# Kernel optimization log

Hardware: AMD Instinct MI355X
Metric: run time of the kernel (lower is better)

## Reference

```python
import jax, jax.numpy as jnp
import numpy as np

N_NODES = 100000
N_EDGES = 1600000
IN_CH = 128
EMB = 64


def _init_linear(key, fan_in, fan_out):
    kw, kb = jax.random.split(key)
    scale = 1.0 / np.sqrt(fan_in)
    W = jax.random.uniform(kw, (fan_in, fan_out), jnp.float32, -scale, scale)
    b = jax.random.uniform(kb, (fan_out,), jnp.float32, -scale, scale)
    return W, b


def setup_inputs() -> dict:
    key = jax.random.key(0)
    ks = jax.random.split(key, 6)
    x = jax.random.normal(ks[0], (N_NODES, IN_CH), jnp.float32)
    edge_index = jax.random.randint(ks[1], (2, N_EDGES), 0, N_NODES)
    batch = jnp.zeros((N_NODES,), jnp.int32)
    # conv1 MLP: in_channels -> 32 -> 64 ; conv2 MLP: 64 -> 64 -> embedding_dim
    W1, b1 = _init_linear(ks[2], IN_CH, 32)
    W2, b2 = _init_linear(ks[3], 32, 64)
    W3, b3 = _init_linear(ks[4], 64, 64)
    W4, b4 = _init_linear(ks[5], 64, EMB)
    return {"x": x, "edge_index": edge_index, "batch": batch,
            "W1": W1, "b1": b1, "W2": W2, "b2": b2,
            "W3": W3, "b3": b3, "W4": W4, "b4": b4}


def _mlp(h, Wa, ba, Wb, bb):
    # PyG MLP: Linear -> act -> Linear (plain last layer)
    return jax.nn.relu(h @ Wa + ba) @ Wb + bb


def _gin_conv(x, src, dst, Wa, ba, Wb, bb):
    # out_i = MLP((1+eps)*x_i + sum_{j->i} x_j), eps = 0 (GINConv default)
    agg = jax.ops.segment_sum(x[src], dst, num_segments=N_NODES)  # [N, d]
    return _mlp(x + agg, Wa, ba, Wb, bb)


def reference(x, edge_index, batch, W1, b1, W2, b2, W3, b3, W4, b4):
    src, dst = edge_index[0], edge_index[1]
    h = jax.nn.relu(_gin_conv(x, src, dst, W1, b1, W2, b2))  # [N, 64]
    h = jax.nn.relu(_gin_conv(h, src, dst, W3, b3, W4, b4))  # [N, EMB]
    # batch is overwritten with zeros in the original forward -> single graph
    pooled = jnp.mean(h, axis=0, keepdims=True)  # [1, EMB]
    return h, pooled
```

## Files before the change

kernel.cpp:

```cpp
#include <hip/hip_runtime.h>

#define NN 100000
#define NE 1600000
#define NLB 128
#define CHUNK (NE / NLB)
#define NB 196
#define BN 512

__device__ __forceinline__ float bf2f(unsigned short u) {
    return __uint_as_float(((unsigned int)u) << 16);
}
__device__ __forceinline__ unsigned short f2bf(float f) {
    unsigned int u = __float_as_uint(f);
    return (unsigned short)((u + 0x7FFFu + ((u >> 16) & 1u)) >> 16);
}

__global__ __launch_bounds__(256) void k_lsort(const int* __restrict__ src,
                                               const int* __restrict__ dst,
                                               int* __restrict__ pairs,
                                               int* __restrict__ tstart,
                                               int* __restrict__ tcnt,
                                               int* __restrict__ btot) {
    __shared__ int cnt[NB];
    __shared__ int sc[256];
    __shared__ int cur[NB];
    int tid = threadIdx.x, blk = blockIdx.x;
    int e0 = blk * CHUNK;
    for (int i = tid; i < NB; i += 256) cnt[i] = 0;
    __syncthreads();
    for (int i = tid; i < CHUNK; i += 256) atomicAdd(&cnt[dst[e0 + i] >> 9], 1);
    __syncthreads();
    sc[tid] = (tid < NB) ? cnt[tid] : 0;
    __syncthreads();
    for (int off = 1; off < 256; off <<= 1) {
        int v = (tid >= off) ? sc[tid - off] : 0;
        __syncthreads();
        sc[tid] += v;
        __syncthreads();
    }
    if (tid < NB) {
        int excl = sc[tid] - cnt[tid];
        cur[tid] = excl;
        tstart[blk * NB + tid] = excl;
        tcnt[blk * NB + tid]   = cnt[tid];
        atomicAdd(&btot[tid], cnt[tid]);
    }
    __syncthreads();
    for (int i = tid; i < CHUNK; i += 256) {
        int d = dst[e0 + i], s = src[e0 + i];
        int p = atomicAdd(&cur[d >> 9], 1);
        pairs[e0 + p] = ((d & (BN - 1)) << 17) | s;
    }
}

__global__ __launch_bounds__(1024) void k_build(const int* __restrict__ pairs,
                                                const int* __restrict__ tstart,
                                                const int* __restrict__ tcnt,
                                                const int* __restrict__ btot,
                                                int* __restrict__ csr,
                                                int* __restrict__ row,
                                                int* __restrict__ rend) {
    __shared__ int segS[NLB], segL[NLB];
    __shared__ int ncnt[BN];
    __shared__ int nbase[BN + 1];
    __shared__ int sc[256];
    __shared__ int sc2[256];
    __shared__ int base_s;
    int tid = threadIdx.x, b = blockIdx.x;

    if (tid < 256) sc2[tid] = (tid < NB) ? btot[tid] : 0;
    __syncthreads();
    for (int off = 1; off < 256; off <<= 1) {
        int v = 0;
        if (tid < 256 && tid >= off) v = sc2[tid - off];
        __syncthreads();
        if (tid < 256) sc2[tid] += v;
        __syncthreads();
    }
    if (tid == 0) base_s = (b == 0) ? 0 : sc2[b - 1];
    if (tid < NLB) {
        segS[tid] = tid * CHUNK + tstart[tid * NB + b];
        segL[tid] = tcnt[tid * NB + b];
    }
    for (int i = tid; i < BN; i += 1024) ncnt[i] = 0;
    __syncthreads();

    int wave = tid >> 6, lane = tid & 63;
    for (int s = wave; s < NLB; s += 16) {
        int st = segS[s], len = segL[s];
        for (int i = lane; i < len; i += 64)
            atomicAdd(&ncnt[pairs[st + i] >> 17], 1);
    }
    __syncthreads();

    int c0 = 0, c1 = 0, tsum = 0;
    if (tid < 256) { c0 = ncnt[2 * tid]; c1 = ncnt[2 * tid + 1]; tsum = c0 + c1; sc[tid] = tsum; }
    __syncthreads();
    for (int off = 1; off < 256; off <<= 1) {
        int v = 0;
        if (tid < 256 && tid >= off) v = sc[tid - off];
        __syncthreads();
        if (tid < 256) sc[tid] += v;
        __syncthreads();
    }
    if (tid < 256) {
        int excl = sc[tid] - tsum;
        nbase[2 * tid]     = excl;
        nbase[2 * tid + 1] = excl + c0;
        if (tid == 255) nbase[BN] = sc[255];
    }
    __syncthreads();

    int base = base_s;
    if (tid < BN) {
        int n = b * BN + tid;
        if (n < NN) { row[n] = base + nbase[tid]; rend[n] = base + nbase[tid + 1]; }
        ncnt[tid] = 0;
    }
    __syncthreads();

    for (int s = wave; s < NLB; s += 16) {
        int st = segS[s], len = segL[s];
        for (int i = lane; i < len; i += 64) {
            int p = pairs[st + i];
            int ln = p >> 17;
            int pos = atomicAdd(&ncnt[ln], 1);
            csr[base + nbase[ln] + pos] = p & 0x1FFFF;
        }
    }
}

__global__ __launch_bounds__(256) void k_gather32(const int* __restrict__ row,
                                                  const int* __restrict__ rend,
                                                  const int* __restrict__ csr,
                                                  const unsigned short* __restrict__ z,
                                                  float* __restrict__ agg) {
    int n = blockIdx.x * 8 + (threadIdx.x >> 5);
    int f = threadIdx.x & 31;
    int j = row[n], e = rend[n];
    float a0 = 0.f, a1 = 0.f, a2 = 0.f, a3 = 0.f;
    for (; j + 3 < e; j += 4) {
        int i0 = csr[j], i1 = csr[j + 1], i2 = csr[j + 2], i3 = csr[j + 3];
        a0 += bf2f(z[(size_t)i0 * 32 + f]);
        a1 += bf2f(z[(size_t)i1 * 32 + f]);
        a2 += bf2f(z[(size_t)i2 * 32 + f]);
        a3 += bf2f(z[(size_t)i3 * 32 + f]);
    }
    for (; j < e; j++) a0 += bf2f(z[(size_t)csr[j] * 32 + f]);
    agg[(size_t)n * 32 + f] = (a0 + a1) + (a2 + a3);
}

__global__ __launch_bounds__(256) void k_gather64(const int* __restrict__ row,
                                                  const int* __restrict__ rend,
                                                  const int* __restrict__ csr,
                                                  const unsigned short* __restrict__ z,
                                                  float* __restrict__ agg) {
    int n = blockIdx.x * 4 + (threadIdx.x >> 6);
    int f = threadIdx.x & 63;
    int j = row[n], e = rend[n];
    float a0 = 0.f, a1 = 0.f, a2 = 0.f, a3 = 0.f;
    for (; j + 3 < e; j += 4) {
        int i0 = csr[j], i1 = csr[j + 1], i2 = csr[j + 2], i3 = csr[j + 3];
        a0 += bf2f(z[(size_t)i0 * 64 + f]);
        a1 += bf2f(z[(size_t)i1 * 64 + f]);
        a2 += bf2f(z[(size_t)i2 * 64 + f]);
        a3 += bf2f(z[(size_t)i3 * 64 + f]);
    }
    for (; j < e; j++) a0 += bf2f(z[(size_t)csr[j] * 64 + f]);
    agg[(size_t)n * 64 + f] = (a0 + a1) + (a2 + a3);
}

__global__ __launch_bounds__(256) void k_lin1(const float* __restrict__ x,
                                              const float* __restrict__ W1,
                                              unsigned short* __restrict__ z1) {
    __shared__ float Ws[128 * 32];
    __shared__ float xs[32][129];
    for (int i = threadIdx.x; i < 1024; i += 256) {
        float4 w = ((const float4*)W1)[i];
        float* d = &Ws[i * 4];
        d[0] = w.x; d[1] = w.y; d[2] = w.z; d[3] = w.w;
    }
    int n_loc = threadIdx.x >> 3;
    int j0    = (threadIdx.x & 7) * 4;
    for (int base = blockIdx.x * 32; base < NN; base += gridDim.x * 32) {
        __syncthreads();
        for (int t = threadIdx.x; t < 1024; t += 256) {
            int n = t >> 5, c = t & 31;
            float4 v = ((const float4*)(x + (size_t)(base + n) * 128))[c];
            float* d = &xs[n][c * 4];
            d[0] = v.x; d[1] = v.y; d[2] = v.z; d[3] = v.w;
        }
        __syncthreads();
        float a0 = 0.f, a1 = 0.f, a2 = 0.f, a3 = 0.f;
        #pragma unroll 8
        for (int k = 0; k < 128; k++) {
            float xv = xs[n_loc][k];
            float4 w = *(const float4*)&Ws[k * 32 + j0];
            a0 = fmaf(xv, w.x, a0); a1 = fmaf(xv, w.y, a1);
            a2 = fmaf(xv, w.z, a2); a3 = fmaf(xv, w.w, a3);
        }
        ushort4 o = { f2bf(a0), f2bf(a1), f2bf(a2), f2bf(a3) };
        *(ushort4*)&z1[(size_t)(base + n_loc) * 32 + j0] = o;
    }
}

__global__ __launch_bounds__(256) void k_mid(const unsigned short* __restrict__ z1,
                                             const float* __restrict__ agg1,
                                             const float* __restrict__ b1,
                                             const float* __restrict__ W2,
                                             const float* __restrict__ b2,
                                             const float* __restrict__ W3,
                                             unsigned short* __restrict__ z2) {
    __shared__ float W2s[32 * 64];
    __shared__ float W3s[64 * 64];
    __shared__ float ts[32][33];
    __shared__ float hs[32 * 68];
    __shared__ float b1s[32], b2s[64];
    for (int i = threadIdx.x; i < 512; i += 256) {
        float4 w = ((const float4*)W2)[i];
        float* d = &W2s[i * 4];
        d[0] = w.x; d[1] = w.y; d[2] = w.z; d[3] = w.w;
    }
    for (int i = threadIdx.x; i < 1024; i += 256) {
        float4 w = ((const float4*)W3)[i];
        float* d = &W3s[i * 4];
        d[0] = w.x; d[1] = w.y; d[2] = w.z; d[3] = w.w;
    }
    if (threadIdx.x < 32) b1s[threadIdx.x] = b1[threadIdx.x];
    if (threadIdx.x >= 64 && threadIdx.x < 128) b2s[threadIdx.x - 64] = b2[threadIdx.x - 64];
    int n2 = threadIdx.x >> 4;
    int j0 = (threadIdx.x & 15) * 4;
    int na = 2 * n2, nb = 2 * n2 + 1;
    for (int base = blockIdx.x * 32; base < NN; base += gridDim.x * 32) {
        __syncthreads();
        #pragma unroll
        for (int r = 0; r < 4; r++) {
            int idx = threadIdx.x + 256 * r;
            int n = idx >> 5, f = idx & 31;
            ts[n][f] = fmaxf(bf2f(z1[(size_t)base * 32 + idx]) + agg1[(size_t)base * 32 + idx] + b1s[f], 0.f);
        }
        __syncthreads();
        {
            float a00=0,a01=0,a02=0,a03=0,a10=0,a11=0,a12=0,a13=0;
            #pragma unroll 8
            for (int k = 0; k < 32; k++) {
                float t0 = ts[na][k], t1 = ts[nb][k];
                float4 w = *(const float4*)&W2s[k * 64 + j0];
                a00=fmaf(t0,w.x,a00); a01=fmaf(t0,w.y,a01); a02=fmaf(t0,w.z,a02); a03=fmaf(t0,w.w,a03);
                a10=fmaf(t1,w.x,a10); a11=fmaf(t1,w.y,a11); a12=fmaf(t1,w.z,a12); a13=fmaf(t1,w.w,a13);
            }
            *(float4*)&hs[na * 68 + j0] = make_float4(fmaxf(a00+b2s[j0],0.f), fmaxf(a01+b2s[j0+1],0.f),
                                                      fmaxf(a02+b2s[j0+2],0.f), fmaxf(a03+b2s[j0+3],0.f));
            *(float4*)&hs[nb * 68 + j0] = make_float4(fmaxf(a10+b2s[j0],0.f), fmaxf(a11+b2s[j0+1],0.f),
                                                      fmaxf(a12+b2s[j0+2],0.f), fmaxf(a13+b2s[j0+3],0.f));
        }
        __syncthreads();
        {
            float a00=0,a01=0,a02=0,a03=0,a10=0,a11=0,a12=0,a13=0;
            #pragma unroll 8
            for (int k = 0; k < 64; k++) {
                float h0 = hs[na * 68 + k], h1 = hs[nb * 68 + k];
                float4 w = *(const float4*)&W3s[k * 64 + j0];
                a00=fmaf(h0,w.x,a00); a01=fmaf(h0,w.y,a01); a02=fmaf(h0,w.z,a02); a03=fmaf(h0,w.w,a03);
                a10=fmaf(h1,w.x,a10); a11=fmaf(h1,w.y,a11); a12=fmaf(h1,w.z,a12); a13=fmaf(h1,w.w,a13);
            }
            ushort4 oa = { f2bf(a00), f2bf(a01), f2bf(a02), f2bf(a03) };
            ushort4 ob = { f2bf(a10), f2bf(a11), f2bf(a12), f2bf(a13) };
            *(ushort4*)&z2[(size_t)(base + na) * 64 + j0] = oa;
            *(ushort4*)&z2[(size_t)(base + nb) * 64 + j0] = ob;
        }
    }
}

__global__ __launch_bounds__(256) void k_final(const unsigned short* __restrict__ z2,
                                               const float* __restrict__ agg2,
                                               const float* __restrict__ b3,
                                               const float* __restrict__ W4,
                                               const float* __restrict__ b4,
                                               float* __restrict__ out,
                                               float* __restrict__ gpool) {
    __shared__ float W4s[64 * 64];
    __shared__ float us[32 * 68];
    __shared__ float b3s[64], b4s[64], pool[64];
    for (int i = threadIdx.x; i < 1024; i += 256) {
        float4 w = ((const float4*)W4)[i];
        float* d = &W4s[i * 4];
        d[0] = w.x; d[1] = w.y; d[2] = w.z; d[3] = w.w;
    }
    if (threadIdx.x < 64) { b3s[threadIdx.x] = b3[threadIdx.x]; pool[threadIdx.x] = 0.f; }
    if (threadIdx.x >= 64 && threadIdx.x < 128) b4s[threadIdx.x - 64] = b4[threadIdx.x - 64];
    int n2 = threadIdx.x >> 4;
    int j0 = (threadIdx.x & 15) * 4;
    int na = 2 * n2, nb = 2 * n2 + 1;
    float p0 = 0.f, p1 = 0.f, p2 = 0.f, p3 = 0.f;
    for (int base = blockIdx.x * 32; base < NN; base += gridDim.x * 32) {
        __syncthreads();
        #pragma unroll
        for (int r = 0; r < 8; r++) {
            int idx = threadIdx.x + 256 * r;
            int n = idx >> 6, f = idx & 63;
            us[n * 68 + f] = fmaxf(bf2f(z2[(size_t)base * 64 + idx]) + agg2[(size_t)base * 64 + idx] + b3s[f], 0.f);
        }
        __syncthreads();
        float a00=0,a01=0,a02=0,a03=0,a10=0,a11=0,a12=0,a13=0;
        #pragma unroll 8
        for (int k = 0; k < 64; k++) {
            float u0 = us[na * 68 + k], u1 = us[nb * 68 + k];
            float4 w = *(const float4*)&W4s[k * 64 + j0];
            a00=fmaf(u0,w.x,a00); a01=fmaf(u0,w.y,a01); a02=fmaf(u0,w.z,a02); a03=fmaf(u0,w.w,a03);
            a10=fmaf(u1,w.x,a10); a11=fmaf(u1,w.y,a11); a12=fmaf(u1,w.z,a12); a13=fmaf(u1,w.w,a13);
        }
        float v00=fmaxf(a00+b4s[j0],0.f), v01=fmaxf(a01+b4s[j0+1],0.f);
        float v02=fmaxf(a02+b4s[j0+2],0.f), v03=fmaxf(a03+b4s[j0+3],0.f);
        float v10=fmaxf(a10+b4s[j0],0.f), v11=fmaxf(a11+b4s[j0+1],0.f);
        float v12=fmaxf(a12+b4s[j0+2],0.f), v13=fmaxf(a13+b4s[j0+3],0.f);
        *(float4*)&out[(size_t)(base + na) * 64 + j0] = make_float4(v00, v01, v02, v03);
        *(float4*)&out[(size_t)(base + nb) * 64 + j0] = make_float4(v10, v11, v12, v13);
        p0 += v00 + v10; p1 += v01 + v11; p2 += v02 + v12; p3 += v03 + v13;
    }
    __syncthreads();
    atomicAdd(&pool[j0 + 0], p0);
    atomicAdd(&pool[j0 + 1], p1);
    atomicAdd(&pool[j0 + 2], p2);
    atomicAdd(&pool[j0 + 3], p3);
    __syncthreads();
    if (threadIdx.x < 64) unsafeAtomicAdd(&gpool[threadIdx.x], pool[threadIdx.x]);
}

__global__ void k_pool(const float* __restrict__ gpool, float* __restrict__ out) {
    int t = threadIdx.x;
    if (t < 64) out[(size_t)NN * 64 + t] = gpool[t] * (1.0f / NN);
}

extern "C" void kernel_launch(void* const* d_in, const int* in_sizes, int n_in,
                              void* d_out, int out_size, void* d_ws, size_t ws_size,
                              hipStream_t stream) {
    const float* x  = (const float*)d_in[0];
    const int*   ei = (const int*)d_in[1];
    const float* W1 = (const float*)d_in[3];
    const float* b1 = (const float*)d_in[4];
    const float* W2 = (const float*)d_in[5];
    const float* b2 = (const float*)d_in[6];
    const float* W3 = (const float*)d_in[7];
    const float* b3 = (const float*)d_in[8];
    const float* W4 = (const float*)d_in[9];
    const float* b4 = (const float*)d_in[10];
    float* out = (float*)d_out;

    int*   ip     = (int*)d_ws;
    int*   tstart = ip;
    int*   tcnt   = ip + NLB * NB;
    int*   btot   = ip + 2 * NLB * NB;
    float* gpool  = (float*)(ip + 2 * NLB * NB + 196);
    int*   row    = ip + 2 * NLB * NB + 260;
    int*   rend   = row + NN;
    int*   csr    = rend + NN;
    int*   pairs  = csr + NE;
    unsigned short* z1b = (unsigned short*)(pairs + NE);
    float* agg1   = (float*)(pairs + NE + NN * 16);
    float* agg2   = (float*)pairs;
    unsigned short* z2b = (unsigned short*)(agg1 + (size_t)NN * 32);
    const int* src = ei;
    const int* dst = ei + NE;

    hipMemsetAsync(btot, 0, (196 + 64) * sizeof(int), stream);
    k_lsort<<<NLB, 256, 0, stream>>>(src, dst, pairs, tstart, tcnt, btot);
    k_build<<<NB, 1024, 0, stream>>>(pairs, tstart, tcnt, btot, csr, row, rend);
    k_lin1<<<1024, 256, 0, stream>>>(x, W1, z1b);
    k_gather32<<<NN / 8, 256, 0, stream>>>(row, rend, csr, z1b, agg1);
    k_mid<<<1024, 256, 0, stream>>>(z1b, agg1, b1, W2, b2, W3, z2b);
    k_gather64<<<NN / 4, 256, 0, stream>>>(row, rend, csr, z2b, agg2);
    k_final<<<1024, 256, 0, stream>>>(z2b, agg2, b3, W4, b4, out, gpool);
    k_pool<<<1, 64, 0, stream>>>(gpool, out);
}
```

Baseline: 352.6 us.

## Fuse edge bucket sort and first linear layer into one launch; unroll gather64

The local edge bucket-sort kernel and the x@W1 projection kernel are merged into a single launch. The first NLB blocks do the sort and the rest do the matmul, so the two independent stages run at the same time on the GPU instead of one after the other. The sort is also split across twice as many blocks (NLB 128→256), which fills more CUs but doubles the per-block offset tables that k_build has to walk. The 64-wide gather loop gains an 8-way unrolled stage to keep more independent loads in flight. The fused kernel carries the larger shared-memory footprint of the matmul in the sort blocks too, which may lower their occupancy.

```diff
diff --git a/kernel.cpp b/kernel.cpp
--- a/kernel.cpp
+++ b/kernel.cpp
@@ -2,7 +2,7 @@
 
 #define NN 100000
 #define NE 1600000
-#define NLB 128
+#define NLB 256
 #define CHUNK (NE / NLB)
 #define NB 196
 #define BN 512
@@ -15,41 +15,78 @@
     return (unsigned short)((u + 0x7FFFu + ((u >> 16) & 1u)) >> 16);
 }
 
-__global__ __launch_bounds__(256) void k_lsort(const int* __restrict__ src,
+__global__ __launch_bounds__(256) void k_front(const int* __restrict__ src,
                                                const int* __restrict__ dst,
                                                int* __restrict__ pairs,
                                                int* __restrict__ tstart,
                                                int* __restrict__ tcnt,
-                                               int* __restrict__ btot) {
+                                               int* __restrict__ btot,
+                                               const float* __restrict__ x,
+                                               const float* __restrict__ W1,
+                                               unsigned short* __restrict__ z1) {
+    __shared__ float Ws[128 * 32];
+    __shared__ float xs[32][129];
     __shared__ int cnt[NB];
     __shared__ int sc[256];
     __shared__ int cur[NB];
-    int tid = threadIdx.x, blk = blockIdx.x;
-    int e0 = blk * CHUNK;
-    for (int i = tid; i < NB; i += 256) cnt[i] = 0;
-    __syncthreads();
-    for (int i = tid; i < CHUNK; i += 256) atomicAdd(&cnt[dst[e0 + i] >> 9], 1);
-    __syncthreads();
-    sc[tid] = (tid < NB) ? cnt[tid] : 0;
-    __syncthreads();
-    for (int off = 1; off < 256; off <<= 1) {
-        int v = (tid >= off) ? sc[tid - off] : 0;
-        __syncthreads();
-        sc[tid] += v;
-        __syncthreads();
-    }
-    if (tid < NB) {
-        int excl = sc[tid] - cnt[tid];
-        cur[tid] = excl;
-        tstart[blk * NB + tid] = excl;
-        tcnt[blk * NB + tid]   = cnt[tid];
-        atomicAdd(&btot[tid], cnt[tid]);
-    }
-    __syncthreads();
-    for (int i = tid; i < CHUNK; i += 256) {
-        int d = dst[e0 + i], s = src[e0 + i];
-        int p = atomicAdd(&cur[d >> 9], 1);
-        pairs[e0 + p] = ((d & (BN - 1)) << 17) | s;
+    int tid = threadIdx.x;
+    if (blockIdx.x < NLB) {
+        int blk = blockIdx.x;
+        int e0 = blk * CHUNK;
+        for (int i = tid; i < NB; i += 256) cnt[i] = 0;
+        __syncthreads();
+        for (int i = tid; i < CHUNK; i += 256) atomicAdd(&cnt[dst[e0 + i] >> 9], 1);
+        __syncthreads();
+        sc[tid] = (tid < NB) ? cnt[tid] : 0;
+        __syncthreads();
+        for (int off = 1; off < 256; off <<= 1) {
+            int v = (tid >= off) ? sc[tid - off] : 0;
+            __syncthreads();
+            sc[tid] += v;
+            __syncthreads();
+        }
+        if (tid < NB) {
+            int excl = sc[tid] - cnt[tid];
+            cur[tid] = excl;
+            tstart[blk * NB + tid] = excl;
+            tcnt[blk * NB + tid]   = cnt[tid];
+            atomicAdd(&btot[tid], cnt[tid]);
+        }
+        __syncthreads();
+        for (int i = tid; i < CHUNK; i += 256) {
+            int d = dst[e0 + i], s = src[e0 + i];
+            int p = atomicAdd(&cur[d >> 9], 1);
+            pairs[e0 + p] = ((d & (BN - 1)) << 17) | s;
+        }
+    } else {
+        int bid = blockIdx.x - NLB;
+        for (int i = tid; i < 1024; i += 256) {
+            float4 w = ((const float4*)W1)[i];
+            float* d = &Ws[i * 4];
+            d[0] = w.x; d[1] = w.y; d[2] = w.z; d[3] = w.w;
+        }
+        int n_loc = tid >> 3;
+        int j0    = (tid & 7) * 4;
+        for (int base = bid * 32; base < NN; base += 1024 * 32) {
+            __syncthreads();
+            for (int t = tid; t < 1024; t += 256) {
+                int n = t >> 5, c = t & 31;
+                float4 v = ((const float4*)(x + (size_t)(base + n) * 128))[c];
+                float* d = &xs[n][c * 4];
+                d[0] = v.x; d[1] = v.y; d[2] = v.z; d[3] = v.w;
+            }
+            __syncthreads();
+            float a0 = 0.f, a1 = 0.f, a2 = 0.f, a3 = 0.f;
+            #pragma unroll 8
+            for (int k = 0; k < 128; k++) {
+                float xv = xs[n_loc][k];
+                float4 w = *(const float4*)&Ws[k * 32 + j0];
+                a0 = fmaf(xv, w.x, a0); a1 = fmaf(xv, w.y, a1);
+                a2 = fmaf(xv, w.z, a2); a3 = fmaf(xv, w.w, a3);
+            }
+            ushort4 o = { f2bf(a0), f2bf(a1), f2bf(a2), f2bf(a3) };
+            *(ushort4*)&z1[(size_t)(base + n_loc) * 32 + j0] = o;
+        }
     }
 }
 
@@ -159,6 +196,19 @@
     int f = threadIdx.x & 63;
     int j = row[n], e = rend[n];
     float a0 = 0.f, a1 = 0.f, a2 = 0.f, a3 = 0.f;
+    for (; j + 7 < e; j += 8) {
+        int i0 = csr[j],     i1 = csr[j + 1], i2 = csr[j + 2], i3 = csr[j + 3];
+        int i4 = csr[j + 4], i5 = csr[j + 5], i6 = csr[j + 6], i7 = csr[j + 7];
+        float v0 = bf2f(z[(size_t)i0 * 64 + f]);
+        float v1 = bf2f(z[(size_t)i1 * 64 + f]);
+        float v2 = bf2f(z[(size_t)i2 * 64 + f]);
+        float v3 = bf2f(z[(size_t)i3 * 64 + f]);
+        float v4 = bf2f(z[(size_t)i4 * 64 + f]);
+        float v5 = bf2f(z[(size_t)i5 * 64 + f]);
+        float v6 = bf2f(z[(size_t)i6 * 64 + f]);
+        float v7 = bf2f(z[(size_t)i7 * 64 + f]);
+        a0 += v0 + v4; a1 += v1 + v5; a2 += v2 + v6; a3 += v3 + v7;
+    }
     for (; j + 3 < e; j += 4) {
         int i0 = csr[j], i1 = csr[j + 1], i2 = csr[j + 2], i3 = csr[j + 3];
         a0 += bf2f(z[(size_t)i0 * 64 + f]);
@@ -168,40 +218,6 @@
     }
     for (; j < e; j++) a0 += bf2f(z[(size_t)csr[j] * 64 + f]);
     agg[(size_t)n * 64 + f] = (a0 + a1) + (a2 + a3);
-}
-
-__global__ __launch_bounds__(256) void k_lin1(const float* __restrict__ x,
-                                              const float* __restrict__ W1,
-                                              unsigned short* __restrict__ z1) {
-    __shared__ float Ws[128 * 32];
-    __shared__ float xs[32][129];
-    for (int i = threadIdx.x; i < 1024; i += 256) {
-        float4 w = ((const float4*)W1)[i];
-        float* d = &Ws[i * 4];
-        d[0] = w.x; d[1] = w.y; d[2] = w.z; d[3] = w.w;
-    }
-    int n_loc = threadIdx.x >> 3;
-    int j0    = (threadIdx.x & 7) * 4;
-    for (int base = blockIdx.x * 32; base < NN; base += gridDim.x * 32) {
-        __syncthreads();
-        for (int t = threadIdx.x; t < 1024; t += 256) {
-            int n = t >> 5, c = t & 31;
-            float4 v = ((const float4*)(x + (size_t)(base + n) * 128))[c];
-            float* d = &xs[n][c * 4];
-            d[0] = v.x; d[1] = v.y; d[2] = v.z; d[3] = v.w;
-        }
-        __syncthreads();
-        float a0 = 0.f, a1 = 0.f, a2 = 0.f, a3 = 0.f;
-        #pragma unroll 8
-        for (int k = 0; k < 128; k++) {
-            float xv = xs[n_loc][k];
-            float4 w = *(const float4*)&Ws[k * 32 + j0];
-            a0 = fmaf(xv, w.x, a0); a1 = fmaf(xv, w.y, a1);
-            a2 = fmaf(xv, w.z, a2); a3 = fmaf(xv, w.w, a3);
-        }
-        ushort4 o = { f2bf(a0), f2bf(a1), f2bf(a2), f2bf(a3) };
-        *(ushort4*)&z1[(size_t)(base + n_loc) * 32 + j0] = o;
-    }
 }
 
 __global__ __launch_bounds__(256) void k_mid(const unsigned short* __restrict__ z1,
@@ -364,9 +380,8 @@
     const int* dst = ei + NE;
 
     hipMemsetAsync(btot, 0, (196 + 64) * sizeof(int), stream);
-    k_lsort<<<NLB, 256, 0, stream>>>(src, dst, pairs, tstart, tcnt, btot);
+    k_front<<<NLB + 1024, 256, 0, stream>>>(src, dst, pairs, tstart, tcnt, btot, x, W1, z1b);
     k_build<<<NB, 1024, 0, stream>>>(pairs, tstart, tcnt, btot, csr, row, rend);
-    k_lin1<<<1024, 256, 0, stream>>>(x, W1, z1b);
     k_gather32<<<NN / 8, 256, 0, stream>>>(row, rend, csr, z1b, agg1);
     k_mid<<<1024, 256, 0, stream>>>(z1b, agg1, b1, W2, b2, W3, z2b);
     k_gather64<<<NN / 4, 256, 0, stream>>>(row, rend, csr, z2b, agg2);
```

New measurement: 326.7 us. 7.4% less time.
